# Kernel optimization log

Measured on AMD Instinct MI355X. Metric: run time of the kernel, lower is better.

The kernel has to match this reference:

```python
import jax, jax.numpy as jnp
import numpy as np

DIM = 1024
HEADS = 16
DIM_HEAD = 64
INNER = HEADS * DIM_HEAD  # 1024


def setup_inputs() -> dict:
    key = jax.random.key(0)
    ks = jax.random.split(key, 6)
    B, N = 4, 2048
    x = jax.random.normal(ks[0], (B, N, DIM), dtype=jnp.float32)
    ln_gamma = jnp.ones((DIM,), jnp.float32)
    ln_beta = jnp.zeros((DIM,), jnp.float32)
    # nn.Linear weights stored [out, in]; apply as x @ W.T
    w_qkv = jax.random.normal(ks[1], (3 * INNER, DIM), dtype=jnp.float32) * (1.0 / np.sqrt(DIM))
    w_out = jax.random.normal(ks[2], (DIM, INNER), dtype=jnp.float32) * (1.0 / np.sqrt(INNER))
    b_out = jax.random.normal(ks[3], (DIM,), dtype=jnp.float32) * 0.01
    return {"x": x, "ln_gamma": ln_gamma, "ln_beta": ln_beta,
            "w_qkv": w_qkv, "w_out": w_out, "b_out": b_out}


def reference(x, ln_gamma, ln_beta, w_qkv, w_out, b_out):
    B, N, _ = x.shape
    scale = DIM_HEAD ** -0.5
    # LayerNorm (eps=1e-5, matching torch default)
    mu = jnp.mean(x, axis=-1, keepdims=True)
    var = jnp.mean(jnp.square(x - mu), axis=-1, keepdims=True)
    xn = (x - mu) * jax.lax.rsqrt(var + 1e-5) * ln_gamma + ln_beta
    qkv = xn @ w_qkv.T  # [B, N, 3*INNER]
    q, k, v = jnp.split(qkv, 3, axis=-1)
    # [B, H, N, Dh]
    def heads(t):
        return t.reshape(B, N, HEADS, DIM_HEAD).transpose(0, 2, 1, 3)
    q, k, v = heads(q), heads(k), heads(v)
    attn = jnp.einsum('bhnd,bhmd->bhnm', q, k) * scale
    attn = jax.nn.softmax(attn, axis=-1)
    out = jnp.einsum('bhnm,bhmd->bhnd', attn, v)
    out = out.transpose(0, 2, 1, 3).reshape(B, N, INNER)
    return out @ w_out.T + b_out
```

## Files before the change

### kernel.cpp

```cpp
#include <hip/hip_runtime.h>

typedef unsigned short u16;
typedef unsigned int u32;
typedef __attribute__((ext_vector_type(8))) short bf16x8;
typedef __attribute__((ext_vector_type(4))) float f32x4;

#define DIM   1024
#define NSEQ  2048
#define BATCH 4
#define HEADS 16
#define DH    64

__device__ __forceinline__ u16 f2bf(float f) {
    unsigned int u = __builtin_bit_cast(unsigned int, f);
    u += 0x7fffu + ((u >> 16) & 1u);
    return (u16)(u >> 16);
}

__device__ __forceinline__ u32 pkbf(float lo, float hi) {
    u32 r;
    asm("v_cvt_pk_bf16_f32 %0, %1, %2" : "=v"(r) : "v"(lo), "v"(hi));
    return r;
}

__device__ __forceinline__ void gload16(const void* g, void* l) {
    __builtin_amdgcn_global_load_lds((__attribute__((address_space(1))) unsigned int*)(g),
                                     (__attribute__((address_space(3))) unsigned int*)(l),
                                     16, 0, 0);
}

#define MFMA16(a, b, c) __builtin_amdgcn_mfma_f32_16x16x32_bf16(a, b, c, 0, 0, 0)

__global__ __launch_bounds__(256) void ln_kernel(const float* __restrict__ x,
                                                 const float* __restrict__ g,
                                                 const float* __restrict__ b,
                                                 u16* __restrict__ xn) {
    int row = blockIdx.x;
    int tid = threadIdx.x;
    const float4 v = ((const float4*)(x + (size_t)row * DIM))[tid];
    float s  = v.x + v.y + v.z + v.w;
    float s2 = v.x * v.x + v.y * v.y + v.z * v.z + v.w * v.w;
#pragma unroll
    for (int o = 32; o; o >>= 1) { s += __shfl_xor(s, o); s2 += __shfl_xor(s2, o); }
    __shared__ float red[8];
    int wid = tid >> 6, lane = tid & 63;
    if (lane == 0) { red[wid] = s; red[4 + wid] = s2; }
    __syncthreads();
    s  = red[0] + red[1] + red[2] + red[3];
    s2 = red[4] + red[5] + red[6] + red[7];
    float mu  = s * (1.0f / DIM);
    float var = s2 * (1.0f / DIM) - mu * mu;
    float rs  = rsqrtf(var + 1e-5f);
    float4 gv = ((const float4*)g)[tid];
    float4 bv = ((const float4*)b)[tid];
    ushort4 o4 = make_ushort4(f2bf((v.x - mu) * rs * gv.x + bv.x),
                              f2bf((v.y - mu) * rs * gv.y + bv.y),
                              f2bf((v.z - mu) * rs * gv.z + bv.z),
                              f2bf((v.w - mu) * rs * gv.w + bv.w));
    ((ushort4*)(xn + (size_t)row * DIM))[tid] = o4;
}

__global__ __launch_bounds__(256) void castw(const float* __restrict__ wqkv,
                                             const float* __restrict__ wout,
                                             u16* __restrict__ wq,
                                             u16* __restrict__ wo) {
    int i = blockIdx.x * 256 + threadIdx.x;
    int e = i * 4;
    if (e < 3 * DIM * DIM) {
        float4 v = *(const float4*)(wqkv + e);
        float sc = (e < DIM * DIM) ? (0.125f * 1.44269504f) : 1.0f;
        *(ushort4*)(wq + e) = make_ushort4(f2bf(v.x * sc), f2bf(v.y * sc),
                                           f2bf(v.z * sc), f2bf(v.w * sc));
    } else {
        int e2 = e - 3 * DIM * DIM;
        float4 v = *(const float4*)(wout + e2);
        *(ushort4*)(wo + e2) = make_ushort4(f2bf(v.x), f2bf(v.y), f2bf(v.z), f2bf(v.w));
    }
}

__global__ __launch_bounds__(256) void gemm_qkv(const u16* __restrict__ A,
                                                const u16* __restrict__ Bw,
                                                u16* __restrict__ qb,
                                                u16* __restrict__ kb,
                                                u16* __restrict__ vtb) {
    __shared__ __align__(16) u16 As[128 * 32];
    __shared__ __align__(16) u16 Bs[128 * 32];
    const int K = DIM;
    int m0 = blockIdx.x * 128, n0 = blockIdx.y * 128;
    int tid = threadIdx.x, lane = tid & 63, wid = tid >> 6;
    int wr = wid >> 1, wc = wid & 1;
    f32x4 acc[4][4] = {};
    for (int k0 = 0; k0 < K; k0 += 32) {
        __syncthreads();
#pragma unroll
        for (int j = 0; j < 2; ++j) {
            int e = j * 256 + tid;
            gload16(A  + (size_t)(m0 + (e >> 2)) * K + k0 + (e & 3) * 8, &As[j * 2048 + wid * 512]);
            gload16(Bw + (size_t)(n0 + (e >> 2)) * K + k0 + (e & 3) * 8, &Bs[j * 2048 + wid * 512]);
        }
        __syncthreads();
        bf16x8 a[4], b[4];
#pragma unroll
        for (int mi = 0; mi < 4; ++mi)
            a[mi] = *(const bf16x8*)&As[(wr * 64 + mi * 16 + (lane & 15)) * 32 + (lane >> 4) * 8];
#pragma unroll
        for (int ni = 0; ni < 4; ++ni)
            b[ni] = *(const bf16x8*)&Bs[(wc * 64 + ni * 16 + (lane & 15)) * 32 + (lane >> 4) * 8];
#pragma unroll
        for (int mi = 0; mi < 4; ++mi)
#pragma unroll
            for (int ni = 0; ni < 4; ++ni)
                acc[mi][ni] = MFMA16(a[mi], b[ni], acc[mi][ni]);
    }
#pragma unroll
    for (int mi = 0; mi < 4; ++mi)
#pragma unroll
        for (int ni = 0; ni < 4; ++ni)
#pragma unroll
            for (int r = 0; r < 4; ++r) {
                int m = m0 + wr * 64 + mi * 16 + (lane >> 4) * 4 + r;
                int n = n0 + wc * 64 + ni * 16 + (lane & 15);
                u16 val = f2bf(acc[mi][ni][r]);
                int part = n >> 10, w = n & 1023, h = w >> 6, d = w & 63;
                int bidx = m >> 11, pos = m & 2047, bh = bidx * HEADS + h;
                if (part == 0)      qb[((size_t)bh * NSEQ + pos) * DH + d] = val;
                else if (part == 1) kb[((size_t)bh * NSEQ + pos) * DH + d] = val;
                else                vtb[((size_t)bh * DH + d) * NSEQ + pos] = val;
            }
}

__global__ __launch_bounds__(512, 4) void attn_kernel(const u16* __restrict__ qb,
                                                      const u16* __restrict__ kb,
                                                      const u16* __restrict__ vtb,
                                                      u16* __restrict__ ob) {
    __shared__ __align__(16) u16 Ks[2][64 * 64];
    __shared__ __align__(16) u16 Vs[2][64 * 64];
    __shared__ __align__(16) u16 Ps[8][2][16 * 64];
    int qt = blockIdx.x, bh = blockIdx.y;
    int tid = threadIdx.x, lane = tid & 63, wid = tid >> 6;
    int q = lane & 15, g = lane >> 4, key = q & 7;

    const size_t kbase = (size_t)bh * NSEQ * DH;
    const size_t vbase = (size_t)bh * DH * NSEQ;

    int sr  = tid >> 3;
    int sc8 = (tid & 7) ^ (sr & 7);

#define STAGE(bi, kv0) do {                                                            \
        gload16(kb  + kbase + (size_t)((kv0) + sr) * DH + sc8 * 8, &Ks[bi][wid * 512]); \
        gload16(vtb + vbase + (size_t)sr * NSEQ + (kv0) + sc8 * 8, &Vs[bi][wid * 512]); \
    } while (0)

    int qbase = qt * 256 + wid * 32;
    bf16x8 aq[2][2];
#pragma unroll
    for (int b = 0; b < 2; ++b) {
        const u16* qp = qb + ((size_t)bh * NSEQ + qbase + b * 16 + q) * DH + 8 * g;
#pragma unroll
        for (int kk = 0; kk < 2; ++kk)
            aq[b][kk] = *(const bf16x8*)(qp + 32 * kk);
    }

    const bf16x8 ones8 = {(short)0x3F80, (short)0x3F80, (short)0x3F80, (short)0x3F80,
                          (short)0x3F80, (short)0x3F80, (short)0x3F80, (short)0x3F80};

    f32x4 oacc[2][4] = {};
    f32x4 lacc[2] = {};

    STAGE(0, 0);
    __syncthreads();

    for (int t = 0; t < 32; ++t) {
        int cur = t & 1;
        if (t < 31) STAGE(1 - cur, (t + 1) * 64);

        f32x4 s[2][4] = {};
#pragma unroll
        for (int nt = 0; nt < 4; ++nt)
#pragma unroll
            for (int kk = 0; kk < 2; ++kk) {
                bf16x8 bk = *(const bf16x8*)&Ks[cur][(nt * 16 + q) * 64 + (((4 * kk + g) ^ key) << 3)];
                s[0][nt] = MFMA16(bk, aq[0][kk], s[0][nt]);
                s[1][nt] = MFMA16(bk, aq[1][kk], s[1][nt]);
            }

#pragma unroll
        for (int b = 0; b < 2; ++b)
#pragma unroll
            for (int nt = 0; nt < 4; ++nt)
#pragma unroll
                for (int i = 0; i < 4; ++i)
                    s[b][nt][i] = exp2f(s[b][nt][i]);

#pragma unroll
        for (int b = 0; b < 2; ++b)
#pragma unroll
            for (int nt = 0; nt < 4; ++nt) {
                uint2 st;
                st.x = pkbf(s[b][nt][0], s[b][nt][1]);
                st.y = pkbf(s[b][nt][2], s[b][nt][3]);
                int w2 = 2 * nt + (g >> 1);
                *(uint2*)&Ps[wid][b][q * 64 + ((w2 ^ key) << 3) + ((g & 1) << 2)] = st;
            }

#pragma unroll
        for (int kk = 0; kk < 2; ++kk) {
            int cbo = ((4 * kk + g) ^ key) << 3;
            bf16x8 pa0 = *(const bf16x8*)&Ps[wid][0][q * 64 + cbo];
            bf16x8 pa1 = *(const bf16x8*)&Ps[wid][1][q * 64 + cbo];
            lacc[0] = MFMA16(pa0, ones8, lacc[0]);
            lacc[1] = MFMA16(pa1, ones8, lacc[1]);
#pragma unroll
            for (int dt = 0; dt < 4; ++dt) {
                bf16x8 vb = *(const bf16x8*)&Vs[cur][(dt * 16 + q) * 64 + cbo];
                oacc[0][dt] = MFMA16(pa0, vb, oacc[0][dt]);
                oacc[1][dt] = MFMA16(pa1, vb, oacc[1][dt]);
            }
        }
        __syncthreads();
    }

    int bb = bh >> 4, h = bh & 15;
#pragma unroll
    for (int b = 0; b < 2; ++b) {
        float iv[4];
#pragma unroll
        for (int i = 0; i < 4; ++i) iv[i] = 1.0f / lacc[b][i];
#pragma unroll
        for (int i = 0; i < 4; ++i) {
            int row = bb * NSEQ + qbase + b * 16 + g * 4 + i;
#pragma unroll
            for (int dt = 0; dt < 4; ++dt)
                ob[(size_t)row * DIM + h * 64 + dt * 16 + q] = f2bf(oacc[b][dt][i] * iv[i]);
        }
    }
#undef STAGE
}

__global__ __launch_bounds__(256) void gemm_out(const u16* __restrict__ A,
                                                const u16* __restrict__ Bw,
                                                const float* __restrict__ bias,
                                                float* __restrict__ out) {
    __shared__ __align__(16) u16 As[128 * 32];
    __shared__ __align__(16) u16 Bs[128 * 32];
    const int K = DIM;
    int m0 = blockIdx.x * 128, n0 = blockIdx.y * 128;
    int tid = threadIdx.x, lane = tid & 63, wid = tid >> 6;
    int wr = wid >> 1, wc = wid & 1;
    f32x4 acc[4][4] = {};
    for (int k0 = 0; k0 < K; k0 += 32) {
        __syncthreads();
#pragma unroll
        for (int j = 0; j < 2; ++j) {
            int e = j * 256 + tid;
            gload16(A  + (size_t)(m0 + (e >> 2)) * K + k0 + (e & 3) * 8, &As[j * 2048 + wid * 512]);
            gload16(Bw + (size_t)(n0 + (e >> 2)) * K + k0 + (e & 3) * 8, &Bs[j * 2048 + wid * 512]);
        }
        __syncthreads();
        bf16x8 a[4], b[4];
#pragma unroll
        for (int mi = 0; mi < 4; ++mi)
            a[mi] = *(const bf16x8*)&As[(wr * 64 + mi * 16 + (lane & 15)) * 32 + (lane >> 4) * 8];
#pragma unroll
        for (int ni = 0; ni < 4; ++ni)
            b[ni] = *(const bf16x8*)&Bs[(wc * 64 + ni * 16 + (lane & 15)) * 32 + (lane >> 4) * 8];
#pragma unroll
        for (int mi = 0; mi < 4; ++mi)
#pragma unroll
            for (int ni = 0; ni < 4; ++ni)
                acc[mi][ni] = MFMA16(a[mi], b[ni], acc[mi][ni]);
    }
#pragma unroll
    for (int mi = 0; mi < 4; ++mi)
#pragma unroll
        for (int ni = 0; ni < 4; ++ni) {
            int n = n0 + wc * 64 + ni * 16 + (lane & 15);
            float bv = bias[n];
#pragma unroll
            for (int r = 0; r < 4; ++r) {
                int m = m0 + wr * 64 + mi * 16 + (lane >> 4) * 4 + r;
                out[(size_t)m * DIM + n] = acc[mi][ni][r] + bv;
            }
        }
}

extern "C" void kernel_launch(void* const* d_in, const int* in_sizes, int n_in,
                              void* d_out, int out_size, void* d_ws, size_t ws_size,
                              hipStream_t stream) {
    const float* x    = (const float*)d_in[0];
    const float* g    = (const float*)d_in[1];
    const float* be   = (const float*)d_in[2];
    const float* wqkv = (const float*)d_in[3];
    const float* wout = (const float*)d_in[4];
    const float* bout = (const float*)d_in[5];
    float* out = (float*)d_out;

    char* ws = (char*)d_ws;
    const size_t MB = 1024u * 1024u;
    u16* xn  = (u16*)(ws);
    u16* wq  = (u16*)(ws + 16 * MB);
    u16* wo  = (u16*)(ws + 22 * MB);
    u16* qb  = (u16*)(ws + 24 * MB);
    u16* kb  = (u16*)(ws + 40 * MB);
    u16* vtb = (u16*)(ws + 56 * MB);
    u16* ao  = xn;

    ln_kernel<<<8192, 256, 0, stream>>>(x, g, be, xn);
    castw<<<4096, 256, 0, stream>>>(wqkv, wout, wq, wo);
    gemm_qkv<<<dim3(64, 24), 256, 0, stream>>>(xn, wq, qb, kb, vtb);
    attn_kernel<<<dim3(8, 64), 512, 0, stream>>>(qb, kb, vtb, ao);
    gemm_out<<<dim3(64, 8), 256, 0, stream>>>(ao, wo, bout, out);
}
```

Measured before the change: 227.6 us.

## Use 32x32 MFMA with transposed S and permlane swap to skip LDS P staging

Attention is restructured around 32x32x16 bf16 MFMAs with S computed transposed (keys x queries), so the exponentiated scores can be packed and rearranged in registers with v_permlane32_swap and fed straight into the PV MFMA as the B operand. This removes the per-wave LDS round trip for P (the Ps buffer and its stores and loads), which also cuts shared memory use. The output is likewise computed transposed, allowing vectorised 8-byte stores per row. The risks are the correctness of the permlane lane mapping, the unchanged lack of max-subtraction in the softmax, and higher VGPR pressure from the f32x16 accumulators under the 512-thread launch bound.

```diff
diff --git a/kernel.cpp b/kernel.cpp
--- a/kernel.cpp
+++ b/kernel.cpp
@@ -4,6 +4,8 @@
 typedef unsigned int u32;
 typedef __attribute__((ext_vector_type(8))) short bf16x8;
 typedef __attribute__((ext_vector_type(4))) float f32x4;
+typedef __attribute__((ext_vector_type(16))) float f32x16;
+typedef __attribute__((ext_vector_type(4))) unsigned int u32x4;
 
 #define DIM   1024
 #define NSEQ  2048
@@ -23,6 +25,10 @@
     return r;
 }
 
+__device__ __forceinline__ void pl32swap(u32& a, u32& b) {
+    asm("v_permlane32_swap_b32 %0, %1" : "+v"(a), "+v"(b));
+}
+
 __device__ __forceinline__ void gload16(const void* g, void* l) {
     __builtin_amdgcn_global_load_lds((__attribute__((address_space(1))) unsigned int*)(g),
                                      (__attribute__((address_space(3))) unsigned int*)(l),
@@ -30,6 +36,7 @@
 }
 
 #define MFMA16(a, b, c) __builtin_amdgcn_mfma_f32_16x16x32_bf16(a, b, c, 0, 0, 0)
+#define MFMA32(a, b, c) __builtin_amdgcn_mfma_f32_32x32x16_bf16(a, b, c, 0, 0, 0)
 
 __global__ __launch_bounds__(256) void ln_kernel(const float* __restrict__ x,
                                                  const float* __restrict__ g,
@@ -135,10 +142,9 @@
                                                       u16* __restrict__ ob) {
     __shared__ __align__(16) u16 Ks[2][64 * 64];
     __shared__ __align__(16) u16 Vs[2][64 * 64];
-    __shared__ __align__(16) u16 Ps[8][2][16 * 64];
     int qt = blockIdx.x, bh = blockIdx.y;
     int tid = threadIdx.x, lane = tid & 63, wid = tid >> 6;
-    int q = lane & 15, g = lane >> 4, key = q & 7;
+    int l31 = lane & 31, hi = lane >> 5, key = l31 & 7;
 
     const size_t kbase = (size_t)bh * NSEQ * DH;
     const size_t vbase = (size_t)bh * DH * NSEQ;
@@ -151,21 +157,18 @@
         gload16(vtb + vbase + (size_t)sr * NSEQ + (kv0) + sc8 * 8, &Vs[bi][wid * 512]); \
     } while (0)
 
-    int qbase = qt * 256 + wid * 32;
-    bf16x8 aq[2][2];
-#pragma unroll
-    for (int b = 0; b < 2; ++b) {
-        const u16* qp = qb + ((size_t)bh * NSEQ + qbase + b * 16 + q) * DH + 8 * g;
-#pragma unroll
-        for (int kk = 0; kk < 2; ++kk)
-            aq[b][kk] = *(const bf16x8*)(qp + 32 * kk);
-    }
+    int qrow = qt * 256 + wid * 32 + l31;
+    const u16* qp = qb + ((size_t)bh * NSEQ + qrow) * DH + 8 * hi;
+    bf16x8 aq[4];
+#pragma unroll
+    for (int kd = 0; kd < 4; ++kd)
+        aq[kd] = *(const bf16x8*)(qp + 16 * kd);
 
     const bf16x8 ones8 = {(short)0x3F80, (short)0x3F80, (short)0x3F80, (short)0x3F80,
                           (short)0x3F80, (short)0x3F80, (short)0x3F80, (short)0x3F80};
 
-    f32x4 oacc[2][4] = {};
-    f32x4 lacc[2] = {};
+    f32x16 oacc[2] = {};
+    f32x16 lacc = {};
 
     STAGE(0, 0);
     __syncthreads();
@@ -174,66 +177,59 @@
         int cur = t & 1;
         if (t < 31) STAGE(1 - cur, (t + 1) * 64);
 
-        f32x4 s[2][4] = {};
-#pragma unroll
-        for (int nt = 0; nt < 4; ++nt)
-#pragma unroll
-            for (int kk = 0; kk < 2; ++kk) {
-                bf16x8 bk = *(const bf16x8*)&Ks[cur][(nt * 16 + q) * 64 + (((4 * kk + g) ^ key) << 3)];
-                s[0][nt] = MFMA16(bk, aq[0][kk], s[0][nt]);
-                s[1][nt] = MFMA16(bk, aq[1][kk], s[1][nt]);
+        f32x16 s[2] = {};
+#pragma unroll
+        for (int kt = 0; kt < 2; ++kt)
+#pragma unroll
+            for (int kd = 0; kd < 4; ++kd) {
+                bf16x8 bk = *(const bf16x8*)&Ks[cur][(kt * 32 + l31) * 64 + (((2 * kd + hi) ^ key) << 3)];
+                s[kt] = MFMA32(bk, aq[kd], s[kt]);
             }
 
 #pragma unroll
-        for (int b = 0; b < 2; ++b)
-#pragma unroll
-            for (int nt = 0; nt < 4; ++nt)
-#pragma unroll
-                for (int i = 0; i < 4; ++i)
-                    s[b][nt][i] = exp2f(s[b][nt][i]);
-
-#pragma unroll
-        for (int b = 0; b < 2; ++b)
-#pragma unroll
-            for (int nt = 0; nt < 4; ++nt) {
-                uint2 st;
-                st.x = pkbf(s[b][nt][0], s[b][nt][1]);
-                st.y = pkbf(s[b][nt][2], s[b][nt][3]);
-                int w2 = 2 * nt + (g >> 1);
-                *(uint2*)&Ps[wid][b][q * 64 + ((w2 ^ key) << 3) + ((g & 1) << 2)] = st;
+        for (int kt = 0; kt < 2; ++kt)
+#pragma unroll
+            for (int i = 0; i < 16; ++i)
+                s[kt][i] = exp2f(s[kt][i]);
+
+#pragma unroll
+        for (int kt = 0; kt < 2; ++kt) {
+            u32 A0 = pkbf(s[kt][0],  s[kt][1]),  B0 = pkbf(s[kt][2],  s[kt][3]);
+            u32 C0 = pkbf(s[kt][4],  s[kt][5]),  D0 = pkbf(s[kt][6],  s[kt][7]);
+            pl32swap(A0, C0); pl32swap(B0, D0);
+            u32x4 wv0 = {A0, B0, C0, D0};
+            bf16x8 pf0 = __builtin_bit_cast(bf16x8, wv0);
+            u32 A1 = pkbf(s[kt][8],  s[kt][9]),  B1 = pkbf(s[kt][10], s[kt][11]);
+            u32 C1 = pkbf(s[kt][12], s[kt][13]), D1 = pkbf(s[kt][14], s[kt][15]);
+            pl32swap(A1, C1); pl32swap(B1, D1);
+            u32x4 wv1 = {A1, B1, C1, D1};
+            bf16x8 pf1 = __builtin_bit_cast(bf16x8, wv1);
+            lacc = MFMA32(ones8, pf0, lacc);
+            lacc = MFMA32(ones8, pf1, lacc);
+#pragma unroll
+            for (int dt = 0; dt < 2; ++dt) {
+                int rbase = (dt * 32 + l31) * 64;
+                bf16x8 vb0 = *(const bf16x8*)&Vs[cur][rbase + (((4 * kt + hi) ^ key) << 3)];
+                oacc[dt] = MFMA32(vb0, pf0, oacc[dt]);
+                bf16x8 vb1 = *(const bf16x8*)&Vs[cur][rbase + (((4 * kt + 2 + hi) ^ key) << 3)];
+                oacc[dt] = MFMA32(vb1, pf1, oacc[dt]);
             }
-
-#pragma unroll
-        for (int kk = 0; kk < 2; ++kk) {
-            int cbo = ((4 * kk + g) ^ key) << 3;
-            bf16x8 pa0 = *(const bf16x8*)&Ps[wid][0][q * 64 + cbo];
-            bf16x8 pa1 = *(const bf16x8*)&Ps[wid][1][q * 64 + cbo];
-            lacc[0] = MFMA16(pa0, ones8, lacc[0]);
-            lacc[1] = MFMA16(pa1, ones8, lacc[1]);
-#pragma unroll
-            for (int dt = 0; dt < 4; ++dt) {
-                bf16x8 vb = *(const bf16x8*)&Vs[cur][(dt * 16 + q) * 64 + cbo];
-                oacc[0][dt] = MFMA16(pa0, vb, oacc[0][dt]);
-                oacc[1][dt] = MFMA16(pa1, vb, oacc[1][dt]);
-            }
         }
         __syncthreads();
     }
 
+    float inv = 1.0f / lacc[0];
     int bb = bh >> 4, h = bh & 15;
-#pragma unroll
-    for (int b = 0; b < 2; ++b) {
-        float iv[4];
-#pragma unroll
-        for (int i = 0; i < 4; ++i) iv[i] = 1.0f / lacc[b][i];
-#pragma unroll
-        for (int i = 0; i < 4; ++i) {
-            int row = bb * NSEQ + qbase + b * 16 + g * 4 + i;
-#pragma unroll
-            for (int dt = 0; dt < 4; ++dt)
-                ob[(size_t)row * DIM + h * 64 + dt * 16 + q] = f2bf(oacc[b][dt][i] * iv[i]);
-        }
-    }
+    u16* orow = ob + ((size_t)(bb * NSEQ + qrow)) * DIM + h * 64 + 4 * hi;
+#pragma unroll
+    for (int dt = 0; dt < 2; ++dt)
+#pragma unroll
+        for (int gg = 0; gg < 4; ++gg) {
+            uint2 st;
+            st.x = pkbf(oacc[dt][4 * gg] * inv,     oacc[dt][4 * gg + 1] * inv);
+            st.y = pkbf(oacc[dt][4 * gg + 2] * inv, oacc[dt][4 * gg + 3] * inv);
+            *(uint2*)(orow + dt * 32 + gg * 8) = st;
+        }
 #undef STAGE
 }
 
```

Result: no change. 229.7 us (+0.9%).
